# Kernel optimization log

Hardware: AMD Instinct MI355X
Metric: run time of the kernel (lower is better)

Reference implementation:

```python
import jax, jax.numpy as jnp
import numpy as np

NUM_NODES = 5  # the 5 ASPP branches form the graph nodes


def conv2d(x, w, b, padding=0, dilation=1):
    # NCHW conv with OIHW kernel, stride 1
    out = jax.lax.conv_general_dilated(
        x, w, window_strides=(1, 1),
        padding=[(padding, padding), (padding, padding)],
        rhs_dilation=(dilation, dilation),
        dimension_numbers=("NCHW", "OIHW", "NCHW"))
    return out + b[None, :, None, None]


def setup_inputs() -> dict:
    key = jax.random.key(0)
    ks = jax.random.split(key, 16)
    Cin, Cmid, Cout = 32, 16, 32
    B, H, W = 8, 384, 384
    s = 0.05
    inp = {
        "x": jax.random.normal(ks[0], (B, Cin, H, W), jnp.float32),
        "w1": jax.random.normal(ks[1], (Cmid, Cin, 1, 1), jnp.float32) * s,
        "b1": jax.random.normal(ks[2], (Cmid,), jnp.float32) * s,
        "w2": jax.random.normal(ks[3], (Cmid, Cin, 3, 3), jnp.float32) * s,
        "b2": jax.random.normal(ks[4], (Cmid,), jnp.float32) * s,
        "w3": jax.random.normal(ks[5], (Cmid, Cin, 3, 3), jnp.float32) * s,
        "b3": jax.random.normal(ks[6], (Cmid,), jnp.float32) * s,
        "w4": jax.random.normal(ks[7], (Cmid, Cin, 3, 3), jnp.float32) * s,
        "b4": jax.random.normal(ks[8], (Cmid,), jnp.float32) * s,
        "w5": jax.random.normal(ks[9], (Cmid, Cin, 1, 1), jnp.float32) * s,
        "b5": jax.random.normal(ks[10], (Cmid,), jnp.float32) * s,
        "gcn_w": jax.random.normal(ks[11], (Cmid, Cmid), jnp.float32) * s,
        "gcn_b": jax.random.normal(ks[12], (Cmid,), jnp.float32) * s,
        "attn_weights": jnp.ones((NUM_NODES,), jnp.float32),
        "fusion_w": jax.random.normal(ks[13], (Cout, Cmid, 1, 1), jnp.float32) * s,
        "fusion_b": jax.random.normal(ks[14], (Cout,), jnp.float32) * s,
    }
    return inp


def reference(x, w1, b1, w2, b2, w3, b3, w4, b4, w5, b5,
              gcn_w, gcn_b, attn_weights, fusion_w, fusion_b):
    # --- ASPP branches ---
    f1 = conv2d(x, w1, b1)                     # 1x1
    f2 = conv2d(x, w2, b2, padding=1, dilation=1)
    f3 = conv2d(x, w3, b3, padding=2, dilation=2)
    f4 = conv2d(x, w4, b4, padding=3, dilation=3)
    gap = x.mean(axis=(2, 3), keepdims=True)   # AdaptiveAvgPool2d(1)
    f5 = conv2d(gap, w5, b5)                   # [B, mid, 1, 1]
    # bilinear upsample of a 1x1 map (align_corners=False) == broadcast
    f5 = jnp.broadcast_to(f5, f1.shape)
    feats = jnp.stack([f1, f2, f3, f4, f5], axis=1)  # [B, 5, mid, H, W]

    # --- node features: per-branch global mean ---
    node_feats = feats.mean(axis=(3, 4))       # [B, 5, mid]

    # --- GCNConv on complete 5-node graph (self-loops added by GCNConv):
    # A_hat = D^{-1/2}(A+I)D^{-1/2} = ones(5,5)/5. Batched over samples.
    A_hat = jnp.full((NUM_NODES, NUM_NODES), 1.0 / NUM_NODES, dtype=x.dtype)
    fused_nodes = jnp.einsum("ij,bjc->bic", A_hat, node_feats @ gcn_w) + gcn_b  # [B,5,mid]

    # --- weighted node fusion ---
    weights = jax.nn.softmax(attn_weights)     # [5]
    out = jnp.einsum("i,bichw,bic->bchw", weights, feats, fused_nodes)  # [B, mid, H, W]

    return conv2d(out, fusion_w, fusion_b)     # [B, out, H, W]
```

## Files before the change

### kernel.cpp

```cpp
#include <hip/hip_runtime.h>
#include <math.h>

#define HH 384
#define WW 384
#define CIN 32
#define HWP (HH*WW)

#define WS_ROWS  0
#define WS_COLSH 1536
#define WS_GSUMH 13824
#define WS_WBF   1536
#define WS_W2    7936
#define WS_CB    12032
#define WS_XBF   16384

typedef __attribute__((ext_vector_type(8))) __bf16 bf16x8;
typedef __attribute__((ext_vector_type(4))) float  f32x4;
typedef __attribute__((ext_vector_type(2))) float  f32x2;

__device__ __forceinline__ unsigned bf16r(float f) {
    unsigned u = __float_as_uint(f);
    return (u + 0x7fffu + ((u >> 16) & 1u)) >> 16;
}

__device__ __forceinline__ unsigned cvt_pk_bf16(float a, float b) {
    unsigned r;
    asm("v_cvt_pk_bf16_f32 %0, %1, %2" : "=v"(r) : "v"(a), "v"(b));
    return r;
}

__device__ __forceinline__ void softmax5(const float* attn, float sw[5]) {
    float a0=attn[0],a1=attn[1],a2=attn[2],a3=attn[3],a4=attn[4];
    float m = fmaxf(fmaxf(fmaxf(a0,a1),fmaxf(a2,a3)),a4);
    float e0=expf(a0-m),e1=expf(a1-m),e2=expf(a2-m),e3=expf(a3-m),e4=expf(a4-m);
    float inv = 1.f/(e0+e1+e2+e3+e4);
    sw[0]=e0*inv; sw[1]=e1*inv; sw[2]=e2*inv; sw[3]=e3*inv; sw[4]=e4*inv;
}

__global__ __launch_bounds__(384) void transform_kernel(const float* __restrict__ x,
        float* __restrict__ ws, unsigned short* __restrict__ xbf) {
    int b = blockIdx.x / HH, h = blockIdx.x % HH;
    int t = threadIdx.x;
    const float* xp = x + (size_t)b*CIN*HWP + (size_t)h*WW + t;

    __shared__ float red[32][100];
    int wv = t >> 6, ln = t & 63;
    int cj = (t < 3) ? t : ((t >= 381) ? t - 378 : -1);
    int sh = h & 7;

    unsigned uu[16];
    #pragma unroll
    for (int ck = 0; ck < 4; ++ck) {
        float v[8];
        #pragma unroll
        for (int j = 0; j < 8; ++j) v[j] = xp[(size_t)(ck*8 + j)*HWP];

        #pragma unroll
        for (int k = 0; k < 4; ++k) uu[ck*4 + k] = cvt_pk_bf16(v[2*k], v[2*k+1]);

        if (cj >= 0) {
            #pragma unroll
            for (int j = 0; j < 8; ++j)
                atomicAdd(&ws[WS_COLSH + (sh*256 + b*32 + ck*8 + j)*6 + cj], v[j]);
        }

        #pragma unroll
        for (int j = 0; j < 8; ++j) {
            float s = v[j];
            s += __shfl_down(s, 32);
            s += __shfl_down(s, 16);
            if (ln < 16) red[ck*8 + j][wv*16 + ln] = s;
        }
    }

    uint4* dst = (uint4*)(xbf + ((size_t)b*HWP + (size_t)h*WW + t)*32);
    dst[0] = make_uint4(uu[0], uu[1], uu[2], uu[3]);
    dst[1] = make_uint4(uu[4], uu[5], uu[6], uu[7]);
    dst[2] = make_uint4(uu[8], uu[9], uu[10], uu[11]);
    dst[3] = make_uint4(uu[12], uu[13], uu[14], uu[15]);

    __syncthreads();
    if (t < 32) {
        f32x4 a4 = {0.f, 0.f, 0.f, 0.f};
        #pragma unroll
        for (int i = 0; i < 24; ++i) a4 += *(const f32x4*)(&red[t][4*i]);
        float rsum = a4[0] + a4[1] + a4[2] + a4[3];
        atomicAdd(&ws[WS_GSUMH + sh*256 + b*32 + t], rsum);
        int rj = (h < 3) ? h : ((h >= 381) ? h - 378 : -1);
        if (rj >= 0) ws[WS_ROWS + (b*32 + t)*6 + rj] = rsum;
    }
}

__device__ __forceinline__ float rectsum(const float* bd, float T, int dh, int dw) {
    int r0 = dh > 0 ?  dh : 0, b0 = dh < 0 ? -dh : 0;
    int c0 = dw > 0 ?  dw : 0, d0 = dw < 0 ? -dw : 0;
    float v = T;
    if (r0) v -= bd[r0-1];
    if (b0) v -= bd[3+b0-1];
    if (c0) v -= bd[6+c0-1];
    if (d0) v -= bd[9+d0-1];
    if (r0 && c0) v += bd[12+(r0-1)*3+(c0-1)];
    if (r0 && d0) v += bd[21+(r0-1)*3+(d0-1)];
    if (b0 && c0) v += bd[30+(b0-1)*3+(c0-1)];
    if (b0 && d0) v += bd[39+(b0-1)*3+(d0-1)];
    return v;
}

__global__ void prep_kernel(const float* __restrict__ x,
                            const float* __restrict__ w1, const float* __restrict__ b1,
                            const float* __restrict__ w2, const float* __restrict__ b2,
                            const float* __restrict__ w3, const float* __restrict__ b3,
                            const float* __restrict__ w4, const float* __restrict__ b4,
                            const float* __restrict__ w5, const float* __restrict__ b5,
                            const float* __restrict__ gcn_w, const float* __restrict__ gcn_b,
                            const float* __restrict__ fusion_w, const float* __restrict__ fusion_b,
                            const float* __restrict__ attn, float* __restrict__ ws) {
    __shared__ float srect[256*28];
    __shared__ float gsum_s[256];
    __shared__ float sacc[128][4];
    __shared__ float ns[128], bbf[128], gl[128];
    float sw[5];
    softmax5(attn, sw);
    int t = threadIdx.x;
    const float invHW = 1.f / (float)HWP;

    {
        float g = 0.f;
        #pragma unroll
        for (int s = 0; s < 8; ++s) g += ws[WS_GSUMH + s*256 + t];
        gsum_s[t] = g;
    }
    __syncthreads();

    {
        int plane = t;
        float bd[48];
        const float* rw = ws + WS_ROWS + plane*6;
        float cl[6];
        #pragma unroll
        for (int j = 0; j < 6; ++j) {
            float s = 0.f;
            #pragma unroll
            for (int sh = 0; sh < 8; ++sh) s += ws[WS_COLSH + (sh*256 + plane)*6 + j];
            cl[j] = s;
        }
        bd[0]=rw[0]; bd[1]=rw[0]+rw[1]; bd[2]=rw[0]+rw[1]+rw[2];
        bd[3]=rw[5]; bd[4]=rw[5]+rw[4]; bd[5]=rw[5]+rw[4]+rw[3];
        bd[6]=cl[0]; bd[7]=cl[0]+cl[1]; bd[8]=cl[0]+cl[1]+cl[2];
        bd[9]=cl[5]; bd[10]=cl[5]+cl[4]; bd[11]=cl[5]+cl[4]+cl[3];
        const float* xp = x + (size_t)plane*HWP;
        for (int a = 1; a <= 3; ++a)
        for (int bb = 1; bb <= 3; ++bb) {
            float tl=0,tr=0,bl=0,br=0;
            for (int h = 0; h < a; ++h)
            for (int w = 0; w < bb; ++w) {
                tl += xp[h*WW + w];
                tr += xp[h*WW + (WW-1-w)];
                bl += xp[(HH-1-h)*WW + w];
                br += xp[(HH-1-h)*WW + (WW-1-w)];
            }
            int o = (a-1)*3 + (bb-1);
            bd[12+o]=tl; bd[21+o]=tr; bd[30+o]=bl; bd[39+o]=br;
        }
        float T = gsum_s[plane];
        float* rp = srect + plane*28;
        #pragma unroll
        for (int d = 0; d < 3; ++d)
        #pragma unroll
        for (int kk = 0; kk < 9; ++kk)
            rp[d*9 + kk] = rectsum(bd, T, (kk/3 - 1)*(d+1), (kk%3 - 1)*(d+1));
        if (t < 128) { sacc[t][0]=0.f; sacc[t][1]=0.f; sacc[t][2]=0.f; sacc[t][3]=0.f; }
    }
    __syncthreads();

    float f5v = 0.f;
    if (t < 128) {
        int b = t >> 4, c = t & 15;
        f5v = b5[c];
        for (int ci = 0; ci < CIN; ++ci)
            f5v += w5[c*CIN+ci] * gsum_s[b*32 + ci] * invHW;
    }
    {
        unsigned short* wbf = (unsigned short*)(ws + WS_WBF);
        const int tk[8] = {0,1,2,3,5,6,7,8};
        for (int idx = t; idx < 25*512; idx += blockDim.x) {
            int tap  = idx >> 9;
            int lane = (idx >> 3) & 63;
            int j    = idx & 7;
            int cin  = ((lane >> 4) << 3) | j;
            int c    = lane & 15;
            float v;
            if (tap == 0) {
                v = sw[0]*w1[c*CIN+cin]
                  + sw[1]*w2[c*288 + cin*9 + 4]
                  + sw[2]*w3[c*288 + cin*9 + 4]
                  + sw[3]*w4[c*288 + cin*9 + 4];
            } else {
                int g = (tap-1) >> 3;
                int mth = (tap-1) & 7;
                int kk = tk[mth];
                const float* w = (g == 0) ? w2 : ((g == 1) ? w3 : w4);
                v = sw[g+1] * w[c*288 + cin*9 + kk];
            }
            wbf[idx] = (unsigned short)bf16r(v);
        }
    }
    __syncthreads();

    {
        int c = t & 15, cing = t >> 4;
        float w1t[2], w2t[2][9], w3t[2][9], w4t[2][9];
        #pragma unroll
        for (int i = 0; i < 2; ++i) {
            int cin = cing*2 + i;
            w1t[i] = w1[c*CIN + cin];
            #pragma unroll
            for (int kk = 0; kk < 9; ++kk) {
                w2t[i][kk] = w2[c*288 + cin*9 + kk];
                w3t[i][kk] = w3[c*288 + cin*9 + kk];
                w4t[i][kk] = w4[c*288 + cin*9 + kk];
            }
        }
        #pragma unroll
        for (int b = 0; b < 8; ++b) {
            float a1 = 0.f, a2 = 0.f, a3 = 0.f, a4 = 0.f;
            #pragma unroll
            for (int i = 0; i < 2; ++i) {
                int plane = b*32 + cing*2 + i;
                const float* rp = srect + plane*28;
                a1 += w1t[i] * gsum_s[plane];
                #pragma unroll
                for (int kk = 0; kk < 9; ++kk) {
                    a2 += w2t[i][kk] * rp[kk];
                    a3 += w3t[i][kk] * rp[9 + kk];
                    a4 += w4t[i][kk] * rp[18 + kk];
                }
            }
            atomicAdd(&sacc[b*16 + c][0], a1);
            atomicAdd(&sacc[b*16 + c][1], a2);
            atomicAdd(&sacc[b*16 + c][2], a3);
            atomicAdd(&sacc[b*16 + c][3], a4);
        }
    }
    __syncthreads();

    if (t < 128) {
        int c = t & 15;
        float nf1 = b1[c] + sacc[t][0]*invHW;
        float nf2 = b2[c] + sacc[t][1]*invHW;
        float nf3 = b3[c] + sacc[t][2]*invHW;
        float nf4 = b4[c] + sacc[t][3]*invHW;
        ns[t]  = 0.2f * (nf1 + nf2 + nf3 + nf4 + f5v);
        bbf[t] = sw[0]*b1[c] + sw[1]*b2[c] + sw[2]*b3[c] + sw[3]*b4[c] + sw[4]*f5v;
    }
    __syncthreads();
    if (t < 128) {
        int b = t >> 4, c = t & 15;
        float acc = gcn_b[c];
        for (int k = 0; k < 16; ++k) acc += ns[b*16 + k] * gcn_w[k*16 + c];
        gl[t] = acc;
    }
    __syncthreads();
    for (int idx = t; idx < 4096; idx += blockDim.x) {
        int b = idx >> 9, c = (idx >> 5) & 15, co = idx & 31;
        ws[WS_W2 + idx] = fusion_w[co*16 + c] * gl[b*16 + c];
    }
    {
        int b = t >> 5, co = t & 31;
        float acc = fusion_b[co];
        for (int c = 0; c < 16; ++c)
            acc += fusion_w[co*16 + c] * gl[b*16 + c] * bbf[b*16 + c];
        ws[WS_CB + t] = acc;
    }
}

__global__ __launch_bounds__(256) void convfuse_kernel(
        const unsigned short* __restrict__ xbf, const unsigned short* __restrict__ wBf,
        const float* __restrict__ ws_ro, float* __restrict__ out) {
    __shared__ __align__(16) char smem[40896];
    unsigned short* sx = (unsigned short*)smem;
    float* w2s = (float*)(smem + 38720);
    float* cbs = (float*)(smem + 40768);
    int blk0 = blockIdx.x;
    int blk = (blk0 & 7) * 576 + (blk0 >> 3);
    int b = blk / 576, tno = blk % 576;
    int h0 = (tno / 24) * 16, w0 = (tno % 24) * 16;
    int tid = threadIdx.x;

    w2s[tid]       = ws_ro[WS_W2 + b*512 + tid];
    w2s[tid + 256] = ws_ro[WS_W2 + b*512 + 256 + tid];
    if (tid < 32) cbs[tid] = ws_ro[WS_CB + b*32 + tid];

    for (int p = tid; p < 484; p += 256) {
        int r = p / 22, c = p - r*22;
        int gh = h0 - 3 + r, gw = w0 - 3 + c;
        uint4 a0 = {0,0,0,0}, a1 = a0, a2 = a0, a3 = a0;
        if ((unsigned)gh < (unsigned)HH && (unsigned)gw < (unsigned)WW) {
            const uint4* src = (const uint4*)(xbf + ((size_t)b*HWP + (size_t)gh*WW + gw)*32);
            a0 = src[0]; a1 = src[1]; a2 = src[2]; a3 = src[3];
        }
        uint4* d = (uint4*)(sx + p*40);
        d[0] = a0; d[1] = a1; d[2] = a2; d[3] = a3;
    }
    __syncthreads();

    int lane = tid & 63, wv = tid >> 6;
    int m = lane & 15, q = lane >> 4;
    int by0 = ((wv*4 + 0 + 3)*22 + 3 + m)*40 + q*8;
    int by1 = by0 + 22*40;
    int by2 = by1 + 22*40;
    int by3 = by2 + 22*40;
    const unsigned short* wfp = wBf + lane*8;

    f32x4 acc0 = {0.f,0.f,0.f,0.f}, acc1 = {0.f,0.f,0.f,0.f};
    f32x4 acc2 = {0.f,0.f,0.f,0.f}, acc3 = {0.f,0.f,0.f,0.f};

    constexpr int TDH[25] = {0, -1,-1,-1,0,0,1,1,1, -2,-2,-2,0,0,2,2,2, -3,-3,-3,0,0,3,3,3};
    constexpr int TDW[25] = {0, -1,0,1,-1,1,-1,0,1, -2,0,2,-2,2,-2,0,2, -3,0,3,-3,3,-3,0,3};
    #pragma unroll
    for (int tap = 0; tap < 25; ++tap) {
        bf16x8 bw = *(const bf16x8*)(wfp + tap*512);
        const int to = (TDH[tap]*22 + TDW[tap])*40;
        acc0 = __builtin_amdgcn_mfma_f32_16x16x32_bf16(*(const bf16x8*)(sx + by0 + to), bw, acc0, 0, 0, 0);
        acc1 = __builtin_amdgcn_mfma_f32_16x16x32_bf16(*(const bf16x8*)(sx + by1 + to), bw, acc1, 0, 0, 0);
        acc2 = __builtin_amdgcn_mfma_f32_16x16x32_bf16(*(const bf16x8*)(sx + by2 + to), bw, acc2, 0, 0, 0);
        acc3 = __builtin_amdgcn_mfma_f32_16x16x32_bf16(*(const bf16x8*)(sx + by3 + to), bw, acc3, 0, 0, 0);
    }
    __syncthreads();

    float* st = (float*)smem;
    #pragma unroll
    for (int g2 = 0; g2 < 4; ++g2) {
        int y = wv*4 + g2;
        f32x4 a = (g2 == 0) ? acc0 : (g2 == 1) ? acc1 : (g2 == 2) ? acc2 : acc3;
        #pragma unroll
        for (int r = 0; r < 4; ++r) {
            int px = q*4 + r;
            st[(y*16 + px)*20 + m] = a[r];
        }
    }
    __syncthreads();

    float sv[16];
    #pragma unroll
    for (int k = 0; k < 4; ++k)
        *(f32x4*)(sv + 4*k) = *(const f32x4*)(st + tid*20 + 4*k);
    f32x2 acc[16];
    #pragma unroll
    for (int co2 = 0; co2 < 16; ++co2) {
        acc[co2][0] = cbs[2*co2];
        acc[co2][1] = cbs[2*co2 + 1];
    }
    #pragma unroll
    for (int c = 0; c < 16; ++c) {
        float v = sv[c];
        #pragma unroll
        for (int co2 = 0; co2 < 16; ++co2) {
            f32x2 w = *(const f32x2*)(w2s + c*32 + 2*co2);
            acc[co2] += w * v;
        }
    }
    int y = tid >> 4, px = tid & 15;
    float* ob = out + (size_t)b*32*HWP + (size_t)(h0 + y)*WW + w0 + px;
    #pragma unroll
    for (int co2 = 0; co2 < 16; ++co2) {
        __builtin_nontemporal_store(acc[co2][0], &ob[(size_t)(2*co2) * HWP]);
        __builtin_nontemporal_store(acc[co2][1], &ob[(size_t)(2*co2 + 1) * HWP]);
    }
}

extern "C" void kernel_launch(void* const* d_in, const int* in_sizes, int n_in,
                              void* d_out, int out_size, void* d_ws, size_t ws_size,
                              hipStream_t stream) {
    const float* x     = (const float*)d_in[0];
    const float* w1    = (const float*)d_in[1];  const float* b1 = (const float*)d_in[2];
    const float* w2    = (const float*)d_in[3];  const float* b2 = (const float*)d_in[4];
    const float* w3    = (const float*)d_in[5];  const float* b3 = (const float*)d_in[6];
    const float* w4    = (const float*)d_in[7];  const float* b4 = (const float*)d_in[8];
    const float* w5    = (const float*)d_in[9];  const float* b5 = (const float*)d_in[10];
    const float* gcn_w = (const float*)d_in[11]; const float* gcn_b = (const float*)d_in[12];
    const float* attn  = (const float*)d_in[13];
    const float* fw    = (const float*)d_in[14]; const float* fb = (const float*)d_in[15];
    float* ws  = (float*)d_ws;
    float* out = (float*)d_out;
    unsigned short* xbf = (unsigned short*)(ws + WS_XBF);

    hipMemsetAsync(ws + WS_COLSH, 0, (15872 - WS_COLSH) * sizeof(float), stream);
    transform_kernel<<<8*HH, 384, 0, stream>>>(x, ws, xbf);
    prep_kernel     <<<1, 256, 0, stream>>>(x, w1,b1,w2,b2,w3,b3,w4,b4,w5,b5,
                                            gcn_w, gcn_b, fw, fb, attn, ws);
    convfuse_kernel <<<4608, 256, 0, stream>>>(xbf, (const unsigned short*)(ws + WS_WBF), ws, out);
}
```

Baseline: 396.4 us.

## Split fused transform into separate reduction and bf16 transpose kernels

Replaces the single pass that converted x to channel-last bf16 while accumulating global, row and column sums via global atomics with two kernels. A stripe-based reduce kernel computes the plane sums and the border row/column partials using vectorized loads and only shared-memory atomics. A simpler transpose kernel then does only the bf16 conversion and store. This removes global atomic contention and shared reduction work from the transpose, at the cost of reading the input tensor twice.

Result: slower. 411.6 us (+3.8%).

```diff
diff --git a/kernel.cpp b/kernel.cpp
--- a/kernel.cpp
+++ b/kernel.cpp
@@ -37,58 +37,88 @@
     sw[0]=e0*inv; sw[1]=e1*inv; sw[2]=e2*inv; sw[3]=e3*inv; sw[4]=e4*inv;
 }
 
-__global__ __launch_bounds__(384) void transform_kernel(const float* __restrict__ x,
-        float* __restrict__ ws, unsigned short* __restrict__ xbf) {
+__global__ __launch_bounds__(256) void reduce_kernel(const float* __restrict__ x,
+        float* __restrict__ ws) {
+    int blk = blockIdx.x;
+    int plane = blk / 6, stripe = blk - plane*6;
+    int t = threadIdx.x;
+    const float* base = x + (size_t)plane*HWP + (size_t)(stripe*64)*WW;
+
+    __shared__ float cols6[6];
+    __shared__ float rowp[3];
+    __shared__ float wsum[4];
+    if (t < 6) cols6[t] = 0.f;
+    if (t < 3) rowp[t] = 0.f;
+    __syncthreads();
+
+    float tot = 0.f;
+    float cl[6] = {0.f,0.f,0.f,0.f,0.f,0.f};
+    bool h0 = false, h95 = false;
+
+    #pragma unroll
+    for (int i = 0; i < 24; ++i) {
+        int f = t + 256*i;
+        f32x4 v = *(const f32x4*)(base + 4*f);
+        float qs = (v[0]+v[1]) + (v[2]+v[3]);
+        tot += qs;
+        int quad = f % 96;
+        if (quad == 0)  { cl[0]+=v[0]; cl[1]+=v[1]; cl[2]+=v[2]; h0 = true; }
+        if (quad == 95) { cl[3]+=v[1]; cl[4]+=v[2]; cl[5]+=v[3]; h95 = true; }
+        if (stripe == 0) {
+            int r = f / 96;
+            if (r < 3) atomicAdd(&rowp[r], qs);
+        } else if (stripe == 5) {
+            int r = f / 96;
+            if (r >= 61) atomicAdd(&rowp[r - 61], qs);
+        }
+    }
+
+    if (h0)  { atomicAdd(&cols6[0], cl[0]); atomicAdd(&cols6[1], cl[1]); atomicAdd(&cols6[2], cl[2]); }
+    if (h95) { atomicAdd(&cols6[3], cl[3]); atomicAdd(&cols6[4], cl[4]); atomicAdd(&cols6[5], cl[5]); }
+
+    #pragma unroll
+    for (int o = 32; o; o >>= 1) tot += __shfl_down(tot, o);
+    int wv = t >> 6, ln = t & 63;
+    if (ln == 0) wsum[wv] = tot;
+    __syncthreads();
+
+    if (t == 0) {
+        float g = (wsum[0]+wsum[1]) + (wsum[2]+wsum[3]);
+        ws[WS_GSUMH + stripe*256 + plane] = g;
+        #pragma unroll
+        for (int j = 0; j < 6; ++j)
+            ws[WS_COLSH + (stripe*256 + plane)*6 + j] = cols6[j];
+        if (stripe == 0) {
+            ws[WS_ROWS + plane*6 + 0] = rowp[0];
+            ws[WS_ROWS + plane*6 + 1] = rowp[1];
+            ws[WS_ROWS + plane*6 + 2] = rowp[2];
+        } else if (stripe == 5) {
+            ws[WS_ROWS + plane*6 + 3] = rowp[0];
+            ws[WS_ROWS + plane*6 + 4] = rowp[1];
+            ws[WS_ROWS + plane*6 + 5] = rowp[2];
+        }
+    }
+}
+
+__global__ __launch_bounds__(384) void transpose_kernel(const float* __restrict__ x,
+        unsigned short* __restrict__ xbf) {
     int b = blockIdx.x / HH, h = blockIdx.x % HH;
     int t = threadIdx.x;
     const float* xp = x + (size_t)b*CIN*HWP + (size_t)h*WW + t;
 
-    __shared__ float red[32][100];
-    int wv = t >> 6, ln = t & 63;
-    int cj = (t < 3) ? t : ((t >= 381) ? t - 378 : -1);
-    int sh = h & 7;
+    float v[32];
+    #pragma unroll
+    for (int ci = 0; ci < 32; ++ci) v[ci] = xp[(size_t)ci*HWP];
 
     unsigned uu[16];
     #pragma unroll
-    for (int ck = 0; ck < 4; ++ck) {
-        float v[8];
-        #pragma unroll
-        for (int j = 0; j < 8; ++j) v[j] = xp[(size_t)(ck*8 + j)*HWP];
-
-        #pragma unroll
-        for (int k = 0; k < 4; ++k) uu[ck*4 + k] = cvt_pk_bf16(v[2*k], v[2*k+1]);
-
-        if (cj >= 0) {
-            #pragma unroll
-            for (int j = 0; j < 8; ++j)
-                atomicAdd(&ws[WS_COLSH + (sh*256 + b*32 + ck*8 + j)*6 + cj], v[j]);
-        }
-
-        #pragma unroll
-        for (int j = 0; j < 8; ++j) {
-            float s = v[j];
-            s += __shfl_down(s, 32);
-            s += __shfl_down(s, 16);
-            if (ln < 16) red[ck*8 + j][wv*16 + ln] = s;
-        }
-    }
+    for (int k = 0; k < 16; ++k) uu[k] = cvt_pk_bf16(v[2*k], v[2*k+1]);
 
     uint4* dst = (uint4*)(xbf + ((size_t)b*HWP + (size_t)h*WW + t)*32);
-    dst[0] = make_uint4(uu[0], uu[1], uu[2], uu[3]);
-    dst[1] = make_uint4(uu[4], uu[5], uu[6], uu[7]);
-    dst[2] = make_uint4(uu[8], uu[9], uu[10], uu[11]);
+    dst[0] = make_uint4(uu[0],  uu[1],  uu[2],  uu[3]);
+    dst[1] = make_uint4(uu[4],  uu[5],  uu[6],  uu[7]);
+    dst[2] = make_uint4(uu[8],  uu[9],  uu[10], uu[11]);
     dst[3] = make_uint4(uu[12], uu[13], uu[14], uu[15]);
-
-    __syncthreads();
-    if (t < 32) {
-        f32x4 a4 = {0.f, 0.f, 0.f, 0.f};
-        #pragma unroll
-        for (int i = 0; i < 24; ++i) a4 += *(const f32x4*)(&red[t][4*i]);
-        float rsum = a4[0] + a4[1] + a4[2] + a4[3];
-        atomicAdd(&ws[WS_GSUMH + sh*256 + b*32 + t], rsum);
-        int rj = (h < 3) ? h : ((h >= 381) ? h - 378 : -1);
-        if (rj >= 0) ws[WS_ROWS + (b*32 + t)*6 + rj] = rsum;
-    }
 }
 
 __device__ __forceinline__ float rectsum(const float* bd, float T, int dh, int dw) {
@@ -386,7 +416,8 @@
     unsigned short* xbf = (unsigned short*)(ws + WS_XBF);
 
     hipMemsetAsync(ws + WS_COLSH, 0, (15872 - WS_COLSH) * sizeof(float), stream);
-    transform_kernel<<<8*HH, 384, 0, stream>>>(x, ws, xbf);
+    reduce_kernel   <<<256*6, 256, 0, stream>>>(x, ws);
+    transpose_kernel<<<8*HH, 384, 0, stream>>>(x, xbf);
     prep_kernel     <<<1, 256, 0, stream>>>(x, w1,b1,w2,b2,w3,b3,w4,b4,w5,b5,
                                             gcn_w, gcn_b, fw, fb, attn, ws);
     convfuse_kernel <<<4608, 256, 0, stream>>>(xbf, (const unsigned short*)(ws + WS_WBF), ws, out);
```
